# Kernel tuning notes

Measured on AMD Instinct MI355X. Metric: run time of the kernel, lower is better.

## Reference

```python
import jax, jax.numpy as jnp
import numpy as np

D_MODEL = 1024
NHEAD = 16
D_K = D_MODEL // NHEAD
CHUNK = 256


def setup_inputs() -> dict:
    key = jax.random.key(0)
    ks = jax.random.split(key, 11)
    S, B = 4096, 4
    inp = {
        "query": jax.random.normal(ks[0], (S, B, D_MODEL), dtype=jnp.float32),
        "key": jax.random.normal(ks[1], (S, B, D_MODEL), dtype=jnp.float32),
        "value": jax.random.normal(ks[2], (S, B, D_MODEL), dtype=jnp.float32),
        # nn.Linear params: y = x @ W.T + b
        "Wq": jax.random.normal(ks[3], (D_MODEL, D_MODEL), dtype=jnp.float32) * 0.02,
        "bq": jnp.zeros((D_MODEL,), dtype=jnp.float32),
        "Wk": jax.random.normal(ks[4], (D_MODEL, D_MODEL), dtype=jnp.float32) * 0.02,
        "bk": jnp.zeros((D_MODEL,), dtype=jnp.float32),
        "Wv": jax.random.normal(ks[5], (D_MODEL, D_MODEL), dtype=jnp.float32) * 0.02,
        "bv": jnp.zeros((D_MODEL,), dtype=jnp.float32),
        "Wo": jax.random.normal(ks[6], (D_MODEL, D_MODEL), dtype=jnp.float32) * 0.02,
        "bo": jnp.zeros((D_MODEL,), dtype=jnp.float32),
    }
    return inp


def _split_heads(x, B):
    # (S, B, D) -> (B, H, S, d_k)
    S = x.shape[0]
    return x.reshape(S, B, NHEAD, D_K).transpose(1, 2, 0, 3)


def reference(query, key, value, Wq, bq, Wk, bk, Wv, bv, Wo, bo):
    S, B, _ = query.shape
    n_chunks = S // CHUNK  # S assumed divisible by CHUNK

    q = _split_heads(query @ Wq.T + bq, B)  # (B,H,S,dk)
    k = _split_heads(key @ Wk.T + bk, B)
    v = _split_heads(value @ Wv.T + bv, B)

    # Block-diagonal attention: softmax is strictly within each chunk.
    qc = q.reshape(B, NHEAD, n_chunks, CHUNK, D_K)
    kc = k.reshape(B, NHEAD, n_chunks, CHUNK, D_K)
    vc = v.reshape(B, NHEAD, n_chunks, CHUNK, D_K)

    scale = 1.0 / np.sqrt(D_K).astype(np.float32)
    scores = jnp.einsum("bhncd,bhnkd->bhnck", qc, kc) * scale  # (B,H,n,C,C)
    probs = jax.nn.softmax(scores, axis=-1)
    out = jnp.einsum("bhnck,bhnkd->bhncd", probs, vc)  # (B,H,n,C,dk)

    # (B,H,S,dk) -> (S,B,H*dk)
    out = out.reshape(B, NHEAD, S, D_K).transpose(2, 0, 1, 3).reshape(S, B, D_MODEL)
    return out @ Wo.T + bo
```

## Files before the change

### kernel.cpp

```cpp
#include <hip/hip_runtime.h>
#include <hip/hip_bf16.h>


namespace {

constexpr int kSeq = 4096, kB = 4, kDm = 1024, kNh = 16, kDk = 64, kChk = 256;
constexpr int kMr = kSeq * kB;
constexpr float kLog2e = 1.44269504088896340736f;

typedef __attribute__((ext_vector_type(8))) short bf16x8;
typedef __attribute__((ext_vector_type(4))) short bf16x4;
typedef __attribute__((ext_vector_type(4))) float f32x4;
typedef __attribute__((ext_vector_type(8))) unsigned short u16x8;
typedef __attribute__((ext_vector_type(4))) unsigned short u16x4;

#define AS1 __attribute__((address_space(1)))
#define AS3 __attribute__((address_space(3)))

__device__ __forceinline__ unsigned short f2bf(float x) {
  union { float f; unsigned u; } v; v.f = x;
  unsigned r = v.u + 0x7fffu + ((v.u >> 16) & 1u);
  return (unsigned short)(r >> 16);
}
__device__ __forceinline__ unsigned cvtpk(float lo, float hi) {
  unsigned r;
  asm("v_cvt_pk_bf16_f32 %0, %1, %2" : "=v"(r) : "v"(lo), "v"(hi));
  return r;
}
__device__ __forceinline__ int swz(int bo) { return bo ^ ((bo >> 3) & 0x70); }

__device__ __forceinline__ f32x4 mfma16x16(bf16x4 a, bf16x4 b, f32x4 c) {
#if __has_builtin(__builtin_amdgcn_mfma_f32_16x16x16bf16_1k)
  return __builtin_amdgcn_mfma_f32_16x16x16bf16_1k(a, b, c, 0, 0, 0);
#else
  asm volatile("v_mfma_f32_16x16x16_bf16 %0, %1, %2, %0\n\ts_nop 4"
               : "+v"(c) : "v"(a), "v"(b));
  return c;
#endif
}

__global__ __launch_bounds__(256) void cvt4(const float* __restrict__ s0,
                                            const float* __restrict__ s1,
                                            const float* __restrict__ s2,
                                            const float* __restrict__ s3,
                                            unsigned short* __restrict__ dst) {
  int i = blockIdx.x * 256 + threadIdx.x;
  int t = i >> 18;
  int j = i & 0x3ffff;
  const float* s = (t == 0) ? s0 : (t == 1) ? s1 : (t == 2) ? s2 : s3;
  f32x4 v = *(const f32x4*)(s + (size_t)j * 4);
  u16x4 o;
  o[0] = f2bf(v[0]); o[1] = f2bf(v[1]); o[2] = f2bf(v[2]); o[3] = f2bf(v[3]);
  *(u16x4*)(dst + (size_t)i * 4) = o;
}

__global__ __launch_bounds__(256) void cvt_all(const float* __restrict__ q,
                                               const float* __restrict__ k,
                                               const float* __restrict__ v,
                                               const float* __restrict__ w0,
                                               const float* __restrict__ w1,
                                               const float* __restrict__ w2,
                                               const float* __restrict__ w3,
                                               unsigned short* __restrict__ wdst,
                                               unsigned short* __restrict__ qkvdst) {
  size_t i = (size_t)blockIdx.x * 256 + threadIdx.x;
  const float* s;
  unsigned short* d;
  size_t j;
  if (i < ((size_t)1 << 20)) {
    int t = (int)(i >> 18); j = i & 0x3ffff;
    s = (t == 0) ? w0 : (t == 1) ? w1 : (t == 2) ? w2 : w3;
    d = wdst + (i << 2);
  } else {
    size_t ii = i - ((size_t)1 << 20);
    int t = (int)(ii >> 22); j = ii & 0x3fffff;
    s = (t == 0) ? q : (t == 1) ? k : v;
    d = qkvdst + (ii << 2);
  }
  f32x4 vv = *(const f32x4*)(s + j * 4);
  u16x4 o;
  o[0] = f2bf(vv[0]); o[1] = f2bf(vv[1]); o[2] = f2bf(vv[2]); o[3] = f2bf(vv[3]);
  *(u16x4*)d = o;
}

__global__ __launch_bounds__(512, 2) void gemm_qkv8(
    const unsigned short* __restrict__ qbf, const unsigned short* __restrict__ kbf,
    const unsigned short* __restrict__ vbf, const unsigned short* __restrict__ Wcat,
    const float* __restrict__ bq, const float* __restrict__ bk,
    const float* __restrict__ bv, unsigned short* __restrict__ dst, float sQ) {
  constexpr int K = kDm, nkt = K / 64;
  __shared__ unsigned short sh[65536];
  const int tid = (int)threadIdx.x;
  const int l = tid & 63;
  const int l15 = l & 15, l4 = l >> 4, l7 = l15 & 7;
  const int wid = tid >> 6, wm = wid >> 2, wn = wid & 3, wn1 = wn & 1;
  const int bid = (int)blockIdx.x;
  const int xcd = bid & 7, idx = bid >> 3;
  const int rbi = xcd * 8 + (idx & 7);
  const int cbi = idx >> 3;
  const int mat = cbi >> 2, ccol = (cbi & 3) * 256;
  const float* bp = (mat == 0) ? bq : (mat == 1) ? bk : bv;
  const float scale = (mat == 0) ? sQ : 1.0f;
  const unsigned short* Ain = (mat == 0) ? qbf : (mat == 1) ? kbf : vbf;
  unsigned short* out = dst + (size_t)mat * kMr * kDm;

  const int srow = tid >> 3;
  const int g16 = (tid & 7) ^ (srow & 7);
  const unsigned short* gA = Ain + (size_t)(rbi * 256 + srow) * K + g16 * 8;
  const unsigned short* gB = Wcat + (size_t)(cbi * 256 + srow) * K + g16 * 8;
  const int ldsbase = (tid & ~63) * 8;

  auto stageA = [&](int T, int h) {
    const unsigned short* s = gA + (size_t)h * (128 * K) + T * 64;
    unsigned short* d = sh + ((T & 1) * 2 + h) * 8192 + ldsbase;
    __builtin_amdgcn_global_load_lds((const AS1 unsigned int*)s, (AS3 unsigned int*)d, 16, 0, 0);
    __builtin_amdgcn_global_load_lds((const AS1 unsigned int*)(s + 64 * K),
                                     (AS3 unsigned int*)(d + 4096), 16, 0, 0);
  };
  auto stageB = [&](int T, int h) {
    const unsigned short* s = gB + (size_t)h * (128 * K) + T * 64;
    unsigned short* d = sh + 32768 + ((T & 1) * 2 + h) * 8192 + ldsbase;
    __builtin_amdgcn_global_load_lds((const AS1 unsigned int*)s, (AS3 unsigned int*)d, 16, 0, 0);
    __builtin_amdgcn_global_load_lds((const AS1 unsigned int*)(s + 64 * K),
                                     (AS3 unsigned int*)(d + 4096), 16, 0, 0);
  };

  f32x4 acc[8][4] = {};
  bf16x8 bfr[4];

  stageB(0, 0); stageB(0, 1);
  stageA(0, 0); stageA(0, 1);
  stageB(1, 0); stageB(1, 1);
  asm volatile("s_waitcnt vmcnt(4)" ::: "memory");
  __builtin_amdgcn_s_barrier();

  for (int it = 0; it < nkt / 2; ++it) {
#pragma unroll
    for (int tt = 0; tt < 2; ++tt) {
      const int T = 2 * it + tt;
      const unsigned short* Asl = sh + ((T & 1) * 2 + wm) * 8192;
      const unsigned short* Bsl = sh + 32768 + ((T & 1) * 2 + (wn >> 1)) * 8192;
#pragma unroll
      for (int p = 0; p < 4; ++p) {
        const int kk = p >> 1, mfh = p & 1;
        bf16x8 af[4];
        const int sc = ((kk * 4 + l4) ^ l7) * 8;
        if (mfh == 0) {
#pragma unroll
          for (int nf = 0; nf < 4; ++nf)
            bfr[nf] = *(const bf16x8*)&Bsl[(wn1 * 64 + nf * 16 + l15) * 64 + sc];
        }
#pragma unroll
        for (int i = 0; i < 4; ++i)
          af[i] = *(const bf16x8*)&Asl[(mfh * 64 + i * 16 + l15) * 64 + sc];
        if (p == 0 && T + 1 < nkt) stageA(T + 1, 0);
        if (p == 1 && T + 1 < nkt) stageA(T + 1, 1);
        if (p == 3 && T + 2 < nkt) { stageB(T + 2, 0); stageB(T + 2, 1); }
        __builtin_amdgcn_s_barrier();
        __builtin_amdgcn_s_setprio(1);
#pragma unroll
        for (int i = 0; i < 4; ++i)
#pragma unroll
          for (int nf = 0; nf < 4; ++nf)
            acc[mfh * 4 + i][nf] =
                __builtin_amdgcn_mfma_f32_16x16x32_bf16(af[i], bfr[nf], acc[mfh * 4 + i][nf], 0, 0, 0);
        __builtin_amdgcn_s_setprio(0);
        if (p == 3 && T + 1 < nkt) {
          if (T + 2 < nkt) asm volatile("s_waitcnt vmcnt(4)" ::: "memory");
          else             asm volatile("s_waitcnt vmcnt(0)" ::: "memory");
        }
        __builtin_amdgcn_s_barrier();
      }
    }
  }

#pragma unroll
  for (int mf = 0; mf < 8; ++mf)
#pragma unroll
    for (int nf = 0; nf < 4; ++nf) {
      int col = wn * 64 + nf * 16 + l15;
      float bvv = bp[ccol + col];
      int grpc = col >> 6;
      int c16 = (col & 63) >> 3, pos = col & 7;
#pragma unroll
      for (int j = 0; j < 4; ++j) {
        int tl = wm * 128 + mf * 16 + l4 * 4 + j;
        int grp = (tl & 3) * 4 + grpc;
        int u = (tl >> 2) * 8 + c16;
        int byte = (grp * 8192 + u * 16 + pos * 2) ^ (((u >> 3) & 7) << 4);
        *(unsigned short*)((char*)sh + byte) = f2bf((acc[mf][nf][j] + bvv) * scale);
      }
    }
  __syncthreads();
  {
    int inner = tid & 31, grp = tid >> 5;
    int b2 = grp >> 2, hl = grp & 3;
    int h = (cbi & 3) * 4 + hl;
    unsigned short* po = out + ((size_t)(b2 * kNh + h) * kSeq + rbi * 64) * kDk;
#pragma unroll
    for (int i = 0; i < 16; ++i) {
      int u = i * 32 + inner;
      int byte = (grp * 8192 + u * 16) ^ (((u >> 3) & 7) << 4);
      u16x8 v = *(const u16x8*)((const char*)sh + byte);
      *(u16x8*)(po + u * 8) = v;
    }
  }
}

__global__ __launch_bounds__(512, 2) void gemm_o8(const unsigned short* __restrict__ Aw,
                                                  const unsigned short* __restrict__ Bw,
                                                  const float* __restrict__ bias,
                                                  float* __restrict__ Cp) {
  constexpr int K = kDm, nkt = K / 64;
  __shared__ unsigned short sh[65536];
  const int tid = (int)threadIdx.x;
  const int l = tid & 63;
  const int l15 = l & 15, l4 = l >> 4, l7 = l15 & 7;
  const int wid = tid >> 6, wm = wid >> 2, wn = wid & 3, wn1 = wn & 1;
  const int bid = (int)blockIdx.x;
  const int xcd = bid & 7, idx = bid >> 3;
  const int rbi = xcd * 8 + (idx & 7);
  const int cbi = idx >> 3;
  const int rb = rbi * 256, cb = cbi * 256;

  const int srow = tid >> 3;
  const int g16 = (tid & 7) ^ (srow & 7);
  size_t abase[2][2];
#pragma unroll
  for (int h = 0; h < 2; ++h)
#pragma unroll
    for (int i = 0; i < 2; ++i) {
      int t = rb + h * 128 + srow + 64 * i;
      abase[h][i] = ((size_t)((t & 3) * kNh) * kSeq + (t >> 2)) * kDk + g16 * 8;
    }
  const unsigned short* gB = Bw + (size_t)(cb + srow) * K + g16 * 8;
  const int ldsbase = (tid & ~63) * 8;

  auto stageA = [&](int T, int h) {
    unsigned short* d = sh + ((T & 1) * 2 + h) * 8192 + ldsbase;
    size_t ko = (size_t)T * ((size_t)kSeq * kDk);
    __builtin_amdgcn_global_load_lds((const AS1 unsigned int*)(Aw + abase[h][0] + ko),
                                     (AS3 unsigned int*)d, 16, 0, 0);
    __builtin_amdgcn_global_load_lds((const AS1 unsigned int*)(Aw + abase[h][1] + ko),
                                     (AS3 unsigned int*)(d + 4096), 16, 0, 0);
  };
  auto stageB = [&](int T, int h) {
    const unsigned short* s = gB + (size_t)h * (128 * K) + T * 64;
    unsigned short* d = sh + 32768 + ((T & 1) * 2 + h) * 8192 + ldsbase;
    __builtin_amdgcn_global_load_lds((const AS1 unsigned int*)s, (AS3 unsigned int*)d, 16, 0, 0);
    __builtin_amdgcn_global_load_lds((const AS1 unsigned int*)(s + 64 * K),
                                     (AS3 unsigned int*)(d + 4096), 16, 0, 0);
  };

  f32x4 acc[8][4] = {};
  bf16x8 bfr[4];

  stageB(0, 0); stageB(0, 1);
  stageA(0, 0); stageA(0, 1);
  stageB(1, 0); stageB(1, 1);
  asm volatile("s_waitcnt vmcnt(4)" ::: "memory");
  __builtin_amdgcn_s_barrier();

  for (int it = 0; it < nkt / 2; ++it) {
#pragma unroll
    for (int tt = 0; tt < 2; ++tt) {
      const int T = 2 * it + tt;
      const unsigned short* Asl = sh + ((T & 1) * 2 + wm) * 8192;
      const unsigned short* Bsl = sh + 32768 + ((T & 1) * 2 + (wn >> 1)) * 8192;
#pragma unroll
      for (int p = 0; p < 4; ++p) {
        const int kk = p >> 1, mfh = p & 1;
        bf16x8 af[4];
        const int sc = ((kk * 4 + l4) ^ l7) * 8;
        if (mfh == 0) {
#pragma unroll
          for (int nf = 0; nf < 4; ++nf)
            bfr[nf] = *(const bf16x8*)&Bsl[(wn1 * 64 + nf * 16 + l15) * 64 + sc];
        }
#pragma unroll
        for (int i = 0; i < 4; ++i)
          af[i] = *(const bf16x8*)&Asl[(mfh * 64 + i * 16 + l15) * 64 + sc];
        if (p == 0 && T + 1 < nkt) stageA(T + 1, 0);
        if (p == 1 && T + 1 < nkt) stageA(T + 1, 1);
        if (p == 3 && T + 2 < nkt) { stageB(T + 2, 0); stageB(T + 2, 1); }
        __builtin_amdgcn_s_barrier();
        __builtin_amdgcn_s_setprio(1);
#pragma unroll
        for (int i = 0; i < 4; ++i)
#pragma unroll
          for (int nf = 0; nf < 4; ++nf)
            acc[mfh * 4 + i][nf] =
                __builtin_amdgcn_mfma_f32_16x16x32_bf16(af[i], bfr[nf], acc[mfh * 4 + i][nf], 0, 0, 0);
        __builtin_amdgcn_s_setprio(0);
        if (p == 3 && T + 1 < nkt) {
          if (T + 2 < nkt) asm volatile("s_waitcnt vmcnt(4)" ::: "memory");
          else             asm volatile("s_waitcnt vmcnt(0)" ::: "memory");
        }
        __builtin_amdgcn_s_barrier();
      }
    }
  }

#pragma unroll
  for (int nf = 0; nf < 4; ++nf) {
    int col = cb + wn * 64 + nf * 16 + l15;
    float bvv = bias[col];
#pragma unroll
    for (int mf = 0; mf < 8; ++mf) {
      int row0 = rb + wm * 128 + mf * 16 + l4 * 4;
#pragma unroll
      for (int j = 0; j < 4; ++j)
        Cp[(size_t)(row0 + j) * kDm + col] = acc[mf][nf][j] + bvv;
    }
  }
}

template <int ALAY, int OHM>
__global__ __launch_bounds__(256) void gemm_bt(const void* __restrict__ Ap,
                                               const unsigned short* __restrict__ Bw,
                                               const float* __restrict__ bias,
                                               void* __restrict__ Cp, float scale) {
  constexpr int K = kDm, N = kDm;
  __shared__ unsigned short As[2][128 * 32];
  __shared__ unsigned short Bs[2][128 * 32];
  const int tid = (int)threadIdx.x;
  const int l = tid & 63;
  const int wbase = tid & ~63;
  const int bid = (int)blockIdx.x;
  const int lin = (bid & 7) * 128 + (bid >> 3);
  const int rb = (lin >> 3) * 128, cb = (lin & 7) * 128;
  const int wr = ((tid >> 7) & 1) * 64;
  const int wc = ((tid >> 6) & 1) * 64;
  const int l15 = l & 15, l4 = l >> 4;

  f32x4 acc[4][4] = {};

  auto stage = [&](int buf, int k0) {
    if constexpr (ALAY == 1) {
      const float* A = (const float*)Ap;
#pragma unroll
      for (int i = 0; i < 4; ++i) {
        int ci = tid + 256 * i;
        int rr = ci >> 3, c4 = ci & 7;
        f32x4 v = *(const f32x4*)(A + (size_t)(rb + rr) * K + (k0 + c4 * 4));
        u16x4 o;
        o[0] = f2bf(v[0]); o[1] = f2bf(v[1]); o[2] = f2bf(v[2]); o[3] = f2bf(v[3]);
        *(u16x4*)&As[buf][rr * 32 + c4 * 4] = o;
      }
    } else {
      const unsigned short* A = (const unsigned short*)Ap;
      int h = k0 >> 6, d0 = k0 & 63;
#pragma unroll
      for (int i = 0; i < 2; ++i) {
        int ch = i * 256 + tid;
        int rr = ch >> 2, cc = ch & 3;
        int t = rb + rr; int s = t >> 2, b2 = t & 3;
        const unsigned short* g =
            A + ((size_t)(b2 * kNh + h) * kSeq + s) * kDk + d0 + cc * 8;
        __builtin_amdgcn_global_load_lds((const AS1 unsigned int*)g,
                                         (AS3 unsigned int*)&As[buf][(i * 256 + wbase) * 8],
                                         16, 0, 0);
      }
    }
#pragma unroll
    for (int i = 0; i < 2; ++i) {
      int ch = i * 256 + tid;
      int rr = ch >> 2, cc = ch & 3;
      const unsigned short* g = Bw + (size_t)(cb + rr) * K + (k0 + cc * 8);
      __builtin_amdgcn_global_load_lds((const AS1 unsigned int*)g,
                                       (AS3 unsigned int*)&Bs[buf][(i * 256 + wbase) * 8],
                                       16, 0, 0);
    }
  };

  stage(0, 0);
  __syncthreads();
  int cur = 0;
  constexpr int nkt = K >> 5;
  for (int kt = 0; kt < nkt; ++kt) {
    if (kt + 1 < nkt) stage(cur ^ 1, (kt + 1) << 5);
    bf16x8 af[4], bfr[4];
#pragma unroll
    for (int m = 0; m < 4; ++m)
      af[m] = *(const bf16x8*)&As[cur][(wr + m * 16 + l15) * 32 + l4 * 8];
#pragma unroll
    for (int n = 0; n < 4; ++n)
      bfr[n] = *(const bf16x8*)&Bs[cur][(wc + n * 16 + l15) * 32 + l4 * 8];
#pragma unroll
    for (int m = 0; m < 4; ++m)
#pragma unroll
      for (int n = 0; n < 4; ++n)
        acc[m][n] = __builtin_amdgcn_mfma_f32_16x16x32_bf16(af[m], bfr[n], acc[m][n], 0, 0, 0);
    __syncthreads();
    cur ^= 1;
  }

#pragma unroll
  for (int n = 0; n < 4; ++n) {
    int col = cb + wc + n * 16 + l15;
    float bvv = bias[col];
    int h = col >> 6, dd = col & 63;
#pragma unroll
    for (int m = 0; m < 4; ++m) {
      int row0 = rb + wr + m * 16 + l4 * 4;
#pragma unroll
      for (int j = 0; j < 4; ++j) {
        float v = acc[m][n][j] + bvv;
        int t = row0 + j;
        if constexpr (OHM) {
          int s = t >> 2, b2 = t & 3;
          ((unsigned short*)Cp)[((size_t)(b2 * kNh + h) * kSeq + s) * kDk + dd] =
              f2bf(v * scale);
        } else {
          ((float*)Cp)[(size_t)t * N + col] = v;
        }
      }
    }
  }
}

__global__ __launch_bounds__(256) void attn_blkdiag(const unsigned short* __restrict__ qw,
                                                    const unsigned short* __restrict__ kw,
                                                    const unsigned short* __restrict__ vw,
                                                    unsigned short* __restrict__ ow) {
  __shared__ unsigned short Kl[64 * 64];
  __shared__ unsigned short Vt[64 * 64];
  const int tid = (int)threadIdx.x;
  const int w = tid >> 6, l = tid & 63;
  const int l15 = l & 15, l4 = l >> 4;
  const int bid0 = (int)blockIdx.x;
  const int bid = (bid0 & 7) * 256 + (bid0 >> 3);
  const int hf = bid & 1, c = (bid >> 1) & 15, bh = bid >> 5;
  const size_t base = ((size_t)bh * kSeq + c * kChk) * kDk;
  const unsigned short* qp = qw + base + (size_t)hf * 128 * kDk;
  const unsigned short* kp = kw + base;
  const unsigned short* vp = vw + base;

  bf16x8 q[2][2];
#pragma unroll
  for (int m = 0; m < 2; ++m)
#pragma unroll
    for (int kk = 0; kk < 2; ++kk)
      q[m][kk] = *(const bf16x8*)(qp + (w * 32 + m * 16 + l15) * 64 + kk * 32 + l4 * 8);

  float mst[2] = {-1e30f, -1e30f}, lst[2] = {0.f, 0.f};
  f32x4 oacc[2][4] = {};

  const int r = tid >> 2, c0 = (tid & 3) * 16;
  u16x8 kr0, kr1, vr0, vr1;
  {
    const unsigned short* kt = kp + tid * 16;
    kr0 = *(const u16x8*)kt; kr1 = *(const u16x8*)(kt + 8);
    const unsigned short* vt = vp + tid * 16;
    vr0 = *(const u16x8*)vt; vr1 = *(const u16x8*)(vt + 8);
  }

  for (int kb = 0; kb < 4; ++kb) {
    __syncthreads();
    {
      int bo = r * 128 + c0 * 2;
      *(u16x8*)((char*)Kl + swz(bo)) = kr0;
      *(u16x8*)((char*)Kl + swz(bo + 16)) = kr1;
#pragma unroll
      for (int j = 0; j < 8; ++j) {
        *(unsigned short*)((char*)Vt + swz((c0 + j) * 128 + r * 2)) = vr0[j];
        *(unsigned short*)((char*)Vt + swz((c0 + 8 + j) * 128 + r * 2)) = vr1[j];
      }
    }
    __syncthreads();
    if (kb < 3) {
      const unsigned short* kt = kp + (kb + 1) * (64 * kDk) + tid * 16;
      kr0 = *(const u16x8*)kt; kr1 = *(const u16x8*)(kt + 8);
      const unsigned short* vt = vp + (kb + 1) * (64 * kDk) + tid * 16;
      vr0 = *(const u16x8*)vt; vr1 = *(const u16x8*)(vt + 8);
    }

    f32x4 sacc[4][2] = {};
    __builtin_amdgcn_s_setprio(1);
#pragma unroll
    for (int kk = 0; kk < 2; ++kk) {
      bf16x8 kf[4];
#pragma unroll
      for (int kn = 0; kn < 4; ++kn) {
        int bo = (kn * 16 + l15) * 128 + (kk * 32 + l4 * 8) * 2;
        kf[kn] = *(const bf16x8*)((const char*)Kl + swz(bo));
      }
#pragma unroll
      for (int kn = 0; kn < 4; ++kn)
#pragma unroll
        for (int m = 0; m < 2; ++m)
          sacc[kn][m] = __builtin_amdgcn_mfma_f32_16x16x32_bf16(kf[kn], q[m][kk], sacc[kn][m], 0, 0, 0);
    }
    __builtin_amdgcn_s_setprio(0);

    unsigned pw[2][4][2];
    float cbq[2][4];
#pragma unroll
    for (int m = 0; m < 2; ++m) {
      float rm = -1e30f;
#pragma unroll
      for (int kn = 0; kn < 4; ++kn)
#pragma unroll
        for (int j = 0; j < 4; ++j) rm = fmaxf(rm, sacc[kn][m][j]);
      rm = fmaxf(rm, __shfl_xor(rm, 16, 64));
      rm = fmaxf(rm, __shfl_xor(rm, 32, 64));
      float mn = fmaxf(mst[m], rm);
      float corr = exp2f(mst[m] - mn);
      mst[m] = mn;
      float rs = 0.f;
#pragma unroll
      for (int kn = 0; kn < 4; ++kn) {
#pragma unroll
        for (int j = 0; j < 4; ++j) {
          float p = exp2f(sacc[kn][m][j] - mn);
          sacc[kn][m][j] = p;
          rs += p;
        }
        pw[m][kn][0] = cvtpk(sacc[kn][m][0], sacc[kn][m][1]);
        pw[m][kn][1] = cvtpk(sacc[kn][m][2], sacc[kn][m][3]);
      }
      rs += __shfl_xor(rs, 16, 64);
      rs += __shfl_xor(rs, 32, 64);
      lst[m] = lst[m] * corr + rs;
#pragma unroll
      for (int j = 0; j < 4; ++j) cbq[m][j] = __shfl(corr, l4 * 4 + j, 64);
#pragma unroll
      for (int n = 0; n < 4; ++n)
#pragma unroll
        for (int j = 0; j < 4; ++j) oacc[m][n][j] *= cbq[m][j];
    }

    __builtin_amdgcn_s_setprio(1);
#pragma unroll
    for (int kn = 0; kn < 4; ++kn) {
      bf16x4 vf[4];
#pragma unroll
      for (int n = 0; n < 4; ++n) {
        int bo = (n * 16 + l15) * 128 + (kn * 16 + l4 * 4) * 2;
        vf[n] = *(const bf16x4*)((const char*)Vt + swz(bo));
      }
#pragma unroll
      for (int m = 0; m < 2; ++m) {
        union { unsigned u[2]; bf16x4 h; } pk;
        pk.u[0] = pw[m][kn][0]; pk.u[1] = pw[m][kn][1];
#pragma unroll
        for (int n = 0; n < 4; ++n)
          oacc[m][n] = mfma16x16(pk.h, vf[n], oacc[m][n]);
      }
    }
    __builtin_amdgcn_s_setprio(0);
  }

  unsigned short* op = ow + base + (size_t)hf * 128 * kDk;
#pragma unroll
  for (int m = 0; m < 2; ++m) {
    float inv = 1.f / lst[m];
#pragma unroll
    for (int j = 0; j < 4; ++j) {
      float ib = __shfl(inv, l4 * 4 + j, 64);
      int srow = w * 32 + m * 16 + l4 * 4 + j;
#pragma unroll
      for (int n = 0; n < 4; ++n)
        op[(size_t)srow * 64 + n * 16 + l15] = f2bf(oacc[m][n][j] * ib);
    }
  }
}

}

extern "C" void kernel_launch(void* const* d_in, const int* in_sizes, int n_in,
                              void* d_out, int out_size, void* d_ws, size_t ws_size,
                              hipStream_t stream) {
  const float* query = (const float*)d_in[0];
  const float* key   = (const float*)d_in[1];
  const float* value = (const float*)d_in[2];
  const float* Wq = (const float*)d_in[3];
  const float* bq = (const float*)d_in[4];
  const float* Wk = (const float*)d_in[5];
  const float* bk = (const float*)d_in[6];
  const float* Wv = (const float*)d_in[7];
  const float* bv = (const float*)d_in[8];
  const float* Wo = (const float*)d_in[9];
  const float* bo = (const float*)d_in[10];

  const float sQ = 0.125f * kLog2e;

  const size_t wsz = (size_t)kDm * kDm;
  const size_t tsz = (size_t)kMr * kDm;
  unsigned short* wsp = (unsigned short*)d_ws;
  unsigned short* wqb = wsp;
  unsigned short* wob = wqb + 3 * wsz;
  unsigned short* qws = wqb + 4 * wsz;
  unsigned short* kws = qws + tsz;
  unsigned short* vws = kws + tsz;
  unsigned short* x0  = vws + tsz;

  const size_t needA = (4 * wsz + 6 * tsz) * 2;
  const size_t needB = (4 * wsz + 4 * tsz) * 2;
  if (ws_size < needB) return;

  if (ws_size >= needA) {
    unsigned short* qbf = x0;
    unsigned short* kbf = qbf + tsz;
    unsigned short* vbf = kbf + tsz;
    unsigned short* aws = qbf;
    cvt_all<<<dim3(53248), dim3(256), 0, stream>>>(query, key, value, Wq, Wk, Wv, Wo,
                                                   wqb, qbf);
    gemm_qkv8<<<dim3(768), dim3(512), 0, stream>>>(qbf, kbf, vbf, wqb, bq, bk, bv, qws, sQ);
    attn_blkdiag<<<dim3(2048), 256, 0, stream>>>(qws, kws, vws, aws);
    gemm_o8<<<dim3(256), dim3(512), 0, stream>>>(aws, wob, bo, (float*)d_out);
  } else {
    unsigned short* aws = x0;
    cvt4<<<dim3(4096), dim3(256), 0, stream>>>(Wq, Wk, Wv, Wo, wqb);
    gemm_bt<1, 1><<<dim3(1024), 256, 0, stream>>>(query, wqb, bq, qws, sQ);
    gemm_bt<1, 1><<<dim3(1024), 256, 0, stream>>>(key,   wqb + wsz, bk, kws, 1.0f);
    gemm_bt<1, 1><<<dim3(1024), 256, 0, stream>>>(value, wqb + 2 * wsz, bv, vws, 1.0f);
    attn_blkdiag<<<dim3(2048), 256, 0, stream>>>(qws, kws, vws, aws);
    gemm_bt<2, 0><<<dim3(1024), 256, 0, stream>>>(aws, wob, bo, d_out, 1.0f);
  }
}
```

Measured before the change: 258.8 us.

## Fuse fp32-to-bf16 activation conversion into QKV GEMM A-tile loading

Removes the separate conversion pass over query/key/value. The QKV GEMM now loads fp32 activations into registers, converts them with packed bf16 conversion, and writes them swizzled into LDS, in place of using direct global-to-LDS loads of pre-converted bf16 data. This avoids writing and re-reading three large bf16 activation buffers. In exchange, the GEMM reads twice the bytes for A, needs more registers, and does synchronous LDS writes inside the pipeline. The epilogue also switches to packed conversion, and the fallback gemm_bt path is deleted.

```diff
diff --git a/kernel.cpp b/kernel.cpp
--- a/kernel.cpp
+++ b/kernel.cpp
@@ -13,6 +13,7 @@
 typedef __attribute__((ext_vector_type(4))) float f32x4;
 typedef __attribute__((ext_vector_type(8))) unsigned short u16x8;
 typedef __attribute__((ext_vector_type(4))) unsigned short u16x4;
+typedef __attribute__((ext_vector_type(4))) unsigned u32x4;
 
 #define AS1 __attribute__((address_space(1)))
 #define AS3 __attribute__((address_space(3)))
@@ -54,38 +55,9 @@
   *(u16x4*)(dst + (size_t)i * 4) = o;
 }
 
-__global__ __launch_bounds__(256) void cvt_all(const float* __restrict__ q,
-                                               const float* __restrict__ k,
-                                               const float* __restrict__ v,
-                                               const float* __restrict__ w0,
-                                               const float* __restrict__ w1,
-                                               const float* __restrict__ w2,
-                                               const float* __restrict__ w3,
-                                               unsigned short* __restrict__ wdst,
-                                               unsigned short* __restrict__ qkvdst) {
-  size_t i = (size_t)blockIdx.x * 256 + threadIdx.x;
-  const float* s;
-  unsigned short* d;
-  size_t j;
-  if (i < ((size_t)1 << 20)) {
-    int t = (int)(i >> 18); j = i & 0x3ffff;
-    s = (t == 0) ? w0 : (t == 1) ? w1 : (t == 2) ? w2 : w3;
-    d = wdst + (i << 2);
-  } else {
-    size_t ii = i - ((size_t)1 << 20);
-    int t = (int)(ii >> 22); j = ii & 0x3fffff;
-    s = (t == 0) ? q : (t == 1) ? k : v;
-    d = qkvdst + (ii << 2);
-  }
-  f32x4 vv = *(const f32x4*)(s + j * 4);
-  u16x4 o;
-  o[0] = f2bf(vv[0]); o[1] = f2bf(vv[1]); o[2] = f2bf(vv[2]); o[3] = f2bf(vv[3]);
-  *(u16x4*)d = o;
-}
-
 __global__ __launch_bounds__(512, 2) void gemm_qkv8(
-    const unsigned short* __restrict__ qbf, const unsigned short* __restrict__ kbf,
-    const unsigned short* __restrict__ vbf, const unsigned short* __restrict__ Wcat,
+    const float* __restrict__ qf, const float* __restrict__ kf,
+    const float* __restrict__ vf, const unsigned short* __restrict__ Wcat,
     const float* __restrict__ bq, const float* __restrict__ bk,
     const float* __restrict__ bv, unsigned short* __restrict__ dst, float sQ) {
   constexpr int K = kDm, nkt = K / 64;
@@ -101,22 +73,19 @@
   const int mat = cbi >> 2, ccol = (cbi & 3) * 256;
   const float* bp = (mat == 0) ? bq : (mat == 1) ? bk : bv;
   const float scale = (mat == 0) ? sQ : 1.0f;
-  const unsigned short* Ain = (mat == 0) ? qbf : (mat == 1) ? kbf : vbf;
+  const float* Ain = (mat == 0) ? qf : (mat == 1) ? kf : vf;
   unsigned short* out = dst + (size_t)mat * kMr * kDm;
 
+  const int arow = tid >> 2;
+  const int ac2 = (tid & 3) * 2;
+  const float* gA = Ain + (size_t)(rbi * 256 + arow) * K + ac2 * 8;
+  const int awc0 = (ac2 ^ (arow & 7)) * 8;
+  const int awc1 = ((ac2 + 1) ^ (arow & 7)) * 8;
   const int srow = tid >> 3;
   const int g16 = (tid & 7) ^ (srow & 7);
-  const unsigned short* gA = Ain + (size_t)(rbi * 256 + srow) * K + g16 * 8;
   const unsigned short* gB = Wcat + (size_t)(cbi * 256 + srow) * K + g16 * 8;
   const int ldsbase = (tid & ~63) * 8;
 
-  auto stageA = [&](int T, int h) {
-    const unsigned short* s = gA + (size_t)h * (128 * K) + T * 64;
-    unsigned short* d = sh + ((T & 1) * 2 + h) * 8192 + ldsbase;
-    __builtin_amdgcn_global_load_lds((const AS1 unsigned int*)s, (AS3 unsigned int*)d, 16, 0, 0);
-    __builtin_amdgcn_global_load_lds((const AS1 unsigned int*)(s + 64 * K),
-                                     (AS3 unsigned int*)(d + 4096), 16, 0, 0);
-  };
   auto stageB = [&](int T, int h) {
     const unsigned short* s = gB + (size_t)h * (128 * K) + T * 64;
     unsigned short* d = sh + 32768 + ((T & 1) * 2 + h) * 8192 + ldsbase;
@@ -124,13 +93,34 @@
     __builtin_amdgcn_global_load_lds((const AS1 unsigned int*)(s + 64 * K),
                                      (AS3 unsigned int*)(d + 4096), 16, 0, 0);
   };
+  auto loadA = [&](f32x4* r, int T, int h) {
+    const float* s = gA + (size_t)h * (128 * K) + T * 64;
+    r[0] = *(const f32x4*)s;
+    r[1] = *(const f32x4*)(s + 4);
+    r[2] = *(const f32x4*)(s + 8);
+    r[3] = *(const f32x4*)(s + 12);
+  };
+  auto writeA = [&](const f32x4* r, int T, int h) {
+    unsigned short* d = sh + ((T & 1) * 2 + h) * 8192 + arow * 64;
+    u32x4 w0 = {cvtpk(r[0][0], r[0][1]), cvtpk(r[0][2], r[0][3]),
+                cvtpk(r[1][0], r[1][1]), cvtpk(r[1][2], r[1][3])};
+    u32x4 w1 = {cvtpk(r[2][0], r[2][1]), cvtpk(r[2][2], r[2][3]),
+                cvtpk(r[3][0], r[3][1]), cvtpk(r[3][2], r[3][3])};
+    *(u32x4*)(d + awc0) = w0;
+    *(u32x4*)(d + awc1) = w1;
+  };
 
   f32x4 acc[8][4] = {};
+  f32x4 aA[4], aB[4];
   bf16x8 bfr[4];
 
+  loadA(aA, 0, 0);
+  loadA(aB, 0, 1);
   stageB(0, 0); stageB(0, 1);
-  stageA(0, 0); stageA(0, 1);
   stageB(1, 0); stageB(1, 1);
+  writeA(aA, 0, 0);
+  writeA(aB, 0, 1);
+  asm volatile("s_waitcnt lgkmcnt(0)" ::: "memory");
   asm volatile("s_waitcnt vmcnt(4)" ::: "memory");
   __builtin_amdgcn_s_barrier();
 
@@ -153,9 +143,21 @@
 #pragma unroll
         for (int i = 0; i < 4; ++i)
           af[i] = *(const bf16x8*)&Asl[(mfh * 64 + i * 16 + l15) * 64 + sc];
-        if (p == 0 && T + 1 < nkt) stageA(T + 1, 0);
-        if (p == 1 && T + 1 < nkt) stageA(T + 1, 1);
-        if (p == 3 && T + 2 < nkt) { stageB(T + 2, 0); stageB(T + 2, 1); }
+        if (p == 0 && T + 1 < nkt) {
+          loadA(aA, T + 1, 0);
+          __builtin_amdgcn_sched_barrier(0);
+        }
+        if (p == 1 && T + 1 < nkt) {
+          loadA(aB, T + 1, 1);
+          __builtin_amdgcn_sched_barrier(0);
+        }
+        if (p == 3) {
+          if (T + 2 < nkt) { stageB(T + 2, 0); stageB(T + 2, 1); }
+          if (T + 1 < nkt) {
+            writeA(aA, T + 1, 0);
+            writeA(aB, T + 1, 1);
+          }
+        }
         __builtin_amdgcn_s_barrier();
         __builtin_amdgcn_s_setprio(1);
 #pragma unroll
@@ -165,10 +167,8 @@
             acc[mfh * 4 + i][nf] =
                 __builtin_amdgcn_mfma_f32_16x16x32_bf16(af[i], bfr[nf], acc[mfh * 4 + i][nf], 0, 0, 0);
         __builtin_amdgcn_s_setprio(0);
-        if (p == 3 && T + 1 < nkt) {
-          if (T + 2 < nkt) asm volatile("s_waitcnt vmcnt(4)" ::: "memory");
-          else             asm volatile("s_waitcnt vmcnt(0)" ::: "memory");
-        }
+        if (p == 3)
+          asm volatile("s_waitcnt lgkmcnt(0)" ::: "memory");
         __builtin_amdgcn_s_barrier();
       }
     }
@@ -182,13 +182,17 @@
       float bvv = bp[ccol + col];
       int grpc = col >> 6;
       int c16 = (col & 63) >> 3, pos = col & 7;
+      unsigned p01 = cvtpk((acc[mf][nf][0] + bvv) * scale, (acc[mf][nf][1] + bvv) * scale);
+      unsigned p23 = cvtpk((acc[mf][nf][2] + bvv) * scale, (acc[mf][nf][3] + bvv) * scale);
+      unsigned short ev[4] = {(unsigned short)p01, (unsigned short)(p01 >> 16),
+                              (unsigned short)p23, (unsigned short)(p23 >> 16)};
 #pragma unroll
       for (int j = 0; j < 4; ++j) {
         int tl = wm * 128 + mf * 16 + l4 * 4 + j;
         int grp = (tl & 3) * 4 + grpc;
         int u = (tl >> 2) * 8 + c16;
         int byte = (grp * 8192 + u * 16 + pos * 2) ^ (((u >> 3) & 7) << 4);
-        *(unsigned short*)((char*)sh + byte) = f2bf((acc[mf][nf][j] + bvv) * scale);
+        *(unsigned short*)((char*)sh + byte) = ev[j];
       }
     }
   __syncthreads();
@@ -311,110 +315,6 @@
 #pragma unroll
       for (int j = 0; j < 4; ++j)
         Cp[(size_t)(row0 + j) * kDm + col] = acc[mf][nf][j] + bvv;
-    }
-  }
-}
-
-template <int ALAY, int OHM>
-__global__ __launch_bounds__(256) void gemm_bt(const void* __restrict__ Ap,
-                                               const unsigned short* __restrict__ Bw,
-                                               const float* __restrict__ bias,
-                                               void* __restrict__ Cp, float scale) {
-  constexpr int K = kDm, N = kDm;
-  __shared__ unsigned short As[2][128 * 32];
-  __shared__ unsigned short Bs[2][128 * 32];
-  const int tid = (int)threadIdx.x;
-  const int l = tid & 63;
-  const int wbase = tid & ~63;
-  const int bid = (int)blockIdx.x;
-  const int lin = (bid & 7) * 128 + (bid >> 3);
-  const int rb = (lin >> 3) * 128, cb = (lin & 7) * 128;
-  const int wr = ((tid >> 7) & 1) * 64;
-  const int wc = ((tid >> 6) & 1) * 64;
-  const int l15 = l & 15, l4 = l >> 4;
-
-  f32x4 acc[4][4] = {};
-
-  auto stage = [&](int buf, int k0) {
-    if constexpr (ALAY == 1) {
-      const float* A = (const float*)Ap;
-#pragma unroll
-      for (int i = 0; i < 4; ++i) {
-        int ci = tid + 256 * i;
-        int rr = ci >> 3, c4 = ci & 7;
-        f32x4 v = *(const f32x4*)(A + (size_t)(rb + rr) * K + (k0 + c4 * 4));
-        u16x4 o;
-        o[0] = f2bf(v[0]); o[1] = f2bf(v[1]); o[2] = f2bf(v[2]); o[3] = f2bf(v[3]);
-        *(u16x4*)&As[buf][rr * 32 + c4 * 4] = o;
-      }
-    } else {
-      const unsigned short* A = (const unsigned short*)Ap;
-      int h = k0 >> 6, d0 = k0 & 63;
-#pragma unroll
-      for (int i = 0; i < 2; ++i) {
-        int ch = i * 256 + tid;
-        int rr = ch >> 2, cc = ch & 3;
-        int t = rb + rr; int s = t >> 2, b2 = t & 3;
-        const unsigned short* g =
-            A + ((size_t)(b2 * kNh + h) * kSeq + s) * kDk + d0 + cc * 8;
-        __builtin_amdgcn_global_load_lds((const AS1 unsigned int*)g,
-                                         (AS3 unsigned int*)&As[buf][(i * 256 + wbase) * 8],
-                                         16, 0, 0);
-      }
-    }
-#pragma unroll
-    for (int i = 0; i < 2; ++i) {
-      int ch = i * 256 + tid;
-      int rr = ch >> 2, cc = ch & 3;
-      const unsigned short* g = Bw + (size_t)(cb + rr) * K + (k0 + cc * 8);
-      __builtin_amdgcn_global_load_lds((const AS1 unsigned int*)g,
-                                       (AS3 unsigned int*)&Bs[buf][(i * 256 + wbase) * 8],
-                                       16, 0, 0);
-    }
-  };
-
-  stage(0, 0);
-  __syncthreads();
-  int cur = 0;
-  constexpr int nkt = K >> 5;
-  for (int kt = 0; kt < nkt; ++kt) {
-    if (kt + 1 < nkt) stage(cur ^ 1, (kt + 1) << 5);
-    bf16x8 af[4], bfr[4];
-#pragma unroll
-    for (int m = 0; m < 4; ++m)
-      af[m] = *(const bf16x8*)&As[cur][(wr + m * 16 + l15) * 32 + l4 * 8];
-#pragma unroll
-    for (int n = 0; n < 4; ++n)
-      bfr[n] = *(const bf16x8*)&Bs[cur][(wc + n * 16 + l15) * 32 + l4 * 8];
-#pragma unroll
-    for (int m = 0; m < 4; ++m)
-#pragma unroll
-      for (int n = 0; n < 4; ++n)
-        acc[m][n] = __builtin_amdgcn_mfma_f32_16x16x32_bf16(af[m], bfr[n], acc[m][n], 0, 0, 0);
-    __syncthreads();
-    cur ^= 1;
-  }
-
-#pragma unroll
-  for (int n = 0; n < 4; ++n) {
-    int col = cb + wc + n * 16 + l15;
-    float bvv = bias[col];
-    int h = col >> 6, dd = col & 63;
-#pragma unroll
-    for (int m = 0; m < 4; ++m) {
-      int row0 = rb + wr + m * 16 + l4 * 4;
-#pragma unroll
-      for (int j = 0; j < 4; ++j) {
-        float v = acc[m][n][j] + bvv;
-        int t = row0 + j;
-        if constexpr (OHM) {
-          int s = t >> 2, b2 = t & 3;
-          ((unsigned short*)Cp)[((size_t)(b2 * kNh + h) * kSeq + s) * kDk + dd] =
-              f2bf(v * scale);
-        } else {
-          ((float*)Cp)[(size_t)t * N + col] = v;
-        }
-      }
     }
   }
 }
@@ -593,29 +493,14 @@
   unsigned short* qws = wqb + 4 * wsz;
   unsigned short* kws = qws + tsz;
   unsigned short* vws = kws + tsz;
-  unsigned short* x0  = vws + tsz;
-
-  const size_t needA = (4 * wsz + 6 * tsz) * 2;
-  const size_t needB = (4 * wsz + 4 * tsz) * 2;
-  if (ws_size < needB) return;
-
-  if (ws_size >= needA) {
-    unsigned short* qbf = x0;
-    unsigned short* kbf = qbf + tsz;
-    unsigned short* vbf = kbf + tsz;
-    unsigned short* aws = qbf;
-    cvt_all<<<dim3(53248), dim3(256), 0, stream>>>(query, key, value, Wq, Wk, Wv, Wo,
-                                                   wqb, qbf);
-    gemm_qkv8<<<dim3(768), dim3(512), 0, stream>>>(qbf, kbf, vbf, wqb, bq, bk, bv, qws, sQ);
-    attn_blkdiag<<<dim3(2048), 256, 0, stream>>>(qws, kws, vws, aws);
-    gemm_o8<<<dim3(256), dim3(512), 0, stream>>>(aws, wob, bo, (float*)d_out);
-  } else {
-    unsigned short* aws = x0;
-    cvt4<<<dim3(4096), dim3(256), 0, stream>>>(Wq, Wk, Wv, Wo, wqb);
-    gemm_bt<1, 1><<<dim3(1024), 256, 0, stream>>>(query, wqb, bq, qws, sQ);
-    gemm_bt<1, 1><<<dim3(1024), 256, 0, stream>>>(key,   wqb + wsz, bk, kws, 1.0f);
-    gemm_bt<1, 1><<<dim3(1024), 256, 0, stream>>>(value, wqb + 2 * wsz, bv, vws, 1.0f);
-    attn_blkdiag<<<dim3(2048), 256, 0, stream>>>(qws, kws, vws, aws);
-    gemm_bt<2, 0><<<dim3(1024), 256, 0, stream>>>(aws, wob, bo, d_out, 1.0f);
-  }
-}
+  unsigned short* aws = vws + tsz;
+
+  const size_t need = (4 * wsz + 4 * tsz) * 2;
+  if (ws_size < need) return;
+
+  cvt4<<<dim3(4096), dim3(256), 0, stream>>>(Wq, Wk, Wv, Wo, wqb);
+  gemm_qkv8<<<dim3(768), dim3(512), 0, stream>>>(query, key, value, wqb,
+                                                 bq, bk, bv, qws, sQ);
+  attn_blkdiag<<<dim3(2048), 256, 0, stream>>>(qws, kws, vws, aws);
+  gemm_o8<<<dim3(256), dim3(512), 0, stream>>>(aws, wob, bo, (float*)d_out);
+}
```

Result: faster. 245.6 us (-5.1%).
